# Kernel tuning notes

Hardware: AMD Instinct MI355X
Metric: run time of the kernel (lower is better)

The kernel has to match this reference:

```python
import jax, jax.numpy as jnp
import numpy as np

B, T, C, H = 4, 4096, 1024, 64

def setup_inputs() -> dict:
    key = jax.random.key(0)
    k1, k2, k3, k4 = jax.random.split(key, 4)
    x = jax.random.normal(k1, (B, T, C), dtype=jnp.float32)
    # Linear(n_embed, head_size, bias=False), stored as [in, out] for x @ W
    s = 1.0 / np.sqrt(C)
    Wq = jax.random.uniform(k2, (C, H), dtype=jnp.float32, minval=-s, maxval=s)
    Wk = jax.random.uniform(k3, (C, H), dtype=jnp.float32, minval=-s, maxval=s)
    Wv = jax.random.uniform(k4, (C, H), dtype=jnp.float32, minval=-s, maxval=s)
    return {"x": x, "Wq": Wq, "Wk": Wk, "Wv": Wv}

def reference(x, Wq, Wk, Wv):
    Bn, Tn, Cn = x.shape
    q = x @ Wq  # [B,T,H]
    k = x @ Wk  # [B,T,H]
    v = x @ Wv  # [B,T,H]
    # NOTE: original scales by C**-0.5 (embedding dim), not head_size**-0.5
    wei = jnp.einsum('bqh,bkh->bqk', q, k) * (Cn ** -0.5)  # [B,T,T]
    causal = jnp.tril(jnp.ones((Tn, Tn), dtype=bool))
    wei = jnp.where(causal, wei, -jnp.inf)
    wei = jax.nn.softmax(wei, axis=-1)
    out = jnp.einsum('bqk,bkh->bqh', wei, v)  # [B,T,H]
    return out
```

## Files before the change

### kernel.cpp

```cpp
#include <hip/hip_runtime.h>
#include <hip/hip_bf16.h>


#define B_DIM 4
#define T_DIM 4096
#define C_DIM 1024
#define H_DIM 64
#define SCALE2 0.0450842066f
#define KP 72

typedef __attribute__((ext_vector_type(8))) short bf8;
typedef __attribute__((ext_vector_type(4))) float f32x4;

__device__ __forceinline__ float fast_exp2(float f) {
    return __builtin_amdgcn_exp2f(f);
}
__device__ __forceinline__ ushort f2bf(float f) {
    union { float f; uint u; } x; x.f = f;
    const uint u = x.u;
    return (ushort)((u + 0x7FFFu + ((u >> 16) & 1u)) >> 16);
}
__device__ __forceinline__ uint cvt_pk_bf16(float lo, float hi) {
    uint r;
    asm("v_cvt_pk_bf16_f32 %0, %1, %2" : "=v"(r) : "v"(lo), "v"(hi));
    return r;
}

__global__ __launch_bounds__(256) void wt_kernel(
    const float* __restrict__ Wq, const float* __restrict__ Wk,
    const float* __restrict__ Wv, ushort* __restrict__ wtg)
{
    const int id  = blockIdx.x * 256 + threadIdx.x;
    const int col = id >> 7;
    const int k8  = (id & 127) * 8;
    const int m   = col >> 6, lc = col & 63;
    const float* W = (m == 0) ? Wq : (m == 1) ? Wk : Wv;
    ushort o[8];
    #pragma unroll
    for (int i = 0; i < 8; ++i)
        o[i] = f2bf(W[(size_t)(k8 + i) * H_DIM + lc]);
    *(bf8*)&wtg[(size_t)col * C_DIM + k8] = *(bf8*)o;
}

__global__ __launch_bounds__(256) void qkv_mfma_kernel(
    const float* __restrict__ x, const ushort* __restrict__ wtg,
    ushort* __restrict__ qo, ushort* __restrict__ ko, ushort* __restrict__ vo)
{
    __shared__ ushort xs[32][KP];
    __shared__ ushort wts[192][KP];
    const int t    = threadIdx.x;
    const int lane = t & 63, wave = t >> 6;
    const int g    = lane >> 4, lid = lane & 15;
    const size_t r0 = (size_t)blockIdx.x * 32;

    f32x4 acc[2][3] = {};

    const int xrow = t >> 3, xcol = (t & 7) * 8;
    float4 xr[2];
    bf8 wreg[6];

    xr[0] = *(const float4*)&x[(r0 + xrow) * C_DIM + xcol];
    xr[1] = *(const float4*)&x[(r0 + xrow) * C_DIM + xcol + 4];
    #pragma unroll
    for (int it = 0; it < 6; ++it) {
        const int n = t + it * 256;
        wreg[it] = *(const bf8*)&wtg[(size_t)(n >> 3) * C_DIM + (n & 7) * 8];
    }

    for (int kc = 0; kc < C_DIM / 64; ++kc) {
        __syncthreads();
        {
            uint p[4];
            p[0] = cvt_pk_bf16(xr[0].x, xr[0].y); p[1] = cvt_pk_bf16(xr[0].z, xr[0].w);
            p[2] = cvt_pk_bf16(xr[1].x, xr[1].y); p[3] = cvt_pk_bf16(xr[1].z, xr[1].w);
            *(bf8*)&xs[xrow][xcol] = *(bf8*)p;
            #pragma unroll
            for (int it = 0; it < 6; ++it) {
                const int n = t + it * 256;
                *(bf8*)&wts[n >> 3][(n & 7) * 8] = wreg[it];
            }
        }
        __syncthreads();
        if (kc + 1 < C_DIM / 64) {
            const int kb = (kc + 1) * 64;
            xr[0] = *(const float4*)&x[(r0 + xrow) * C_DIM + kb + xcol];
            xr[1] = *(const float4*)&x[(r0 + xrow) * C_DIM + kb + xcol + 4];
            #pragma unroll
            for (int it = 0; it < 6; ++it) {
                const int n = t + it * 256;
                wreg[it] = *(const bf8*)&wtg[(size_t)(n >> 3) * C_DIM + kb + (n & 7) * 8];
            }
        }
        #pragma unroll
        for (int ks = 0; ks < 2; ++ks) {
            const bf8 a0 = *(const bf8*)&xs[lid][ks * 32 + g * 8];
            const bf8 a1 = *(const bf8*)&xs[16 + lid][ks * 32 + g * 8];
            #pragma unroll
            for (int j = 0; j < 3; ++j) {
                const int ct = wave * 3 + j;
                const bf8 bb = *(const bf8*)&wts[ct * 16 + lid][ks * 32 + g * 8];
                acc[0][j] = __builtin_amdgcn_mfma_f32_16x16x32_bf16(a0, bb, acc[0][j], 0, 0, 0);
                acc[1][j] = __builtin_amdgcn_mfma_f32_16x16x32_bf16(a1, bb, acc[1][j], 0, 0, 0);
            }
        }
    }

    #pragma unroll
    for (int rt = 0; rt < 2; ++rt)
        #pragma unroll
        for (int j = 0; j < 3; ++j) {
            const int ct = wave * 3 + j;
            const int m  = ct >> 2, lc = (ct & 3) * 16 + lid;
            ushort* dst = (m == 0) ? qo : (m == 1) ? ko : vo;
            const float sc = (m == 0) ? SCALE2 : 1.f;
            #pragma unroll
            for (int r = 0; r < 4; ++r) {
                const size_t row = r0 + rt * 16 + 4 * g + r;
                dst[row * H_DIM + lc] = f2bf(acc[rt][j][r] * sc);
            }
        }
}

__global__ __launch_bounds__(256) void flash_mfma_kernel(
    const ushort* __restrict__ q, const ushort* __restrict__ k,
    const ushort* __restrict__ v, float* __restrict__ pO,
    float* __restrict__ pm, float* __restrict__ pl,
    float* __restrict__ out, int S, int nslots, int direct)
{
    const int qt = 63 - blockIdx.y;
    const int c  = blockIdx.x;
    const int kt_begin = c * S;
    const int kt_end   = min((c + 1) * S, qt + 1);
    if (kt_begin >= kt_end) return;

    __shared__ ushort ks[64][KP];
    __shared__ ushort vt[64][KP];
    __shared__ ushort ps[4][16][KP];

    const int t    = threadIdx.x;
    const int lane = t & 63, wave = t >> 6;
    const int g    = lane >> 4, lid = lane & 15;
    const int b    = blockIdx.z;
    const int bq0  = qt * 64;
    const size_t base = (size_t)b * T_DIM * H_DIM;

    const size_t qoff = base + (size_t)(bq0 + wave * 16 + lid) * H_DIM;
    const bf8 qf0 = *(const bf8*)&q[qoff + g * 8];
    const bf8 qf1 = *(const bf8*)&q[qoff + 32 + g * 8];

    f32x4 o_acc[4] = {};
    float m_run = -1e30f, l_run = 0.f;

    const int krow = t >> 3, kcol = (t & 7) * 8;
    const int vj = (t & 31) * 2, vc = (t >> 5) * 8;
    bf8 kr0, kr1, vr0, vr1;
    {
        const int kg = kt_begin * 64;
        kr0 = *(const bf8*)&k[base + (size_t)(kg + krow) * H_DIM + kcol];
        kr1 = *(const bf8*)&k[base + (size_t)(kg + 32 + krow) * H_DIM + kcol];
        vr0 = *(const bf8*)&v[base + (size_t)(kg + vj) * H_DIM + vc];
        vr1 = *(const bf8*)&v[base + (size_t)(kg + vj + 1) * H_DIM + vc];
    }

    for (int kt64 = kt_begin; kt64 < kt_end; ++kt64) {
        __syncthreads();
        *(bf8*)&ks[krow][kcol]      = kr0;
        *(bf8*)&ks[32 + krow][kcol] = kr1;
        #pragma unroll
        for (int i = 0; i < 8; ++i) {
            const uint pk = (uint)(ushort)vr0[i] | ((uint)(ushort)vr1[i] << 16);
            *(uint*)&vt[vc + i][vj] = pk;
        }
        __syncthreads();
        if (kt64 + 1 < kt_end) {
            const int kg = (kt64 + 1) * 64;
            kr0 = *(const bf8*)&k[base + (size_t)(kg + krow) * H_DIM + kcol];
            kr1 = *(const bf8*)&k[base + (size_t)(kg + 32 + krow) * H_DIM + kcol];
            vr0 = *(const bf8*)&v[base + (size_t)(kg + vj) * H_DIM + vc];
            vr1 = *(const bf8*)&v[base + (size_t)(kg + vj + 1) * H_DIM + vc];
        }

        f32x4 st[4];
        #pragma unroll
        for (int kt = 0; kt < 4; ++kt) {
            const bf8 kf0 = *(const bf8*)&ks[kt * 16 + lid][g * 8];
            const bf8 kf1 = *(const bf8*)&ks[kt * 16 + lid][32 + g * 8];
            f32x4 a = {0.f, 0.f, 0.f, 0.f};
            a = __builtin_amdgcn_mfma_f32_16x16x32_bf16(kf0, qf0, a, 0, 0, 0);
            a = __builtin_amdgcn_mfma_f32_16x16x32_bf16(kf1, qf1, a, 0, 0, 0);
            st[kt] = a;
        }

        if (kt64 == qt) {
            const int qloc = wave * 16 + lid;
            #pragma unroll
            for (int kt = 0; kt < 4; ++kt)
                #pragma unroll
                for (int r = 0; r < 4; ++r)
                    if (kt * 16 + 4 * g + r > qloc) st[kt][r] = -1e30f;
        }

        float mx = fmaxf(fmaxf(fmaxf(st[0][0], st[0][1]), fmaxf(st[0][2], st[0][3])),
                   fmaxf(fmaxf(fmaxf(st[1][0], st[1][1]), fmaxf(st[1][2], st[1][3])),
                   fmaxf(fmaxf(fmaxf(st[2][0], st[2][1]), fmaxf(st[2][2], st[2][3])),
                         fmaxf(fmaxf(st[3][0], st[3][1]), fmaxf(st[3][2], st[3][3])))));
        mx = fmaxf(mx, __shfl_xor(mx, 16));
        mx = fmaxf(mx, __shfl_xor(mx, 32));
        const bool nof = (mx <= m_run + 8.0f);
        const float mnew = nof ? m_run : mx;
        const float fsc  = nof ? 1.0f : fast_exp2(m_run - mnew);
        m_run = mnew;
        float ls = 0.f;
        #pragma unroll
        for (int kt = 0; kt < 4; ++kt)
            #pragma unroll
            for (int r = 0; r < 4; ++r) {
                const float p = fast_exp2(st[kt][r] - mnew);
                st[kt][r] = p;
                ls += p;
            }
        ls += __shfl_xor(ls, 16);
        ls += __shfl_xor(ls, 32);
        l_run = l_run * fsc + ls;

        #pragma unroll
        for (int kt = 0; kt < 4; ++kt) {
            uint2 w;
            w.x = cvt_pk_bf16(st[kt][0], st[kt][1]);
            w.y = cvt_pk_bf16(st[kt][2], st[kt][3]);
            *(uint2*)&ps[wave][lid][kt * 16 + 4 * g] = w;
        }

        if (!__all(nof)) {
            float fb[4];
            #pragma unroll
            for (int r = 0; r < 4; ++r) fb[r] = __shfl(fsc, 4 * g + r);
            #pragma unroll
            for (int ht = 0; ht < 4; ++ht)
                #pragma unroll
                for (int r = 0; r < 4; ++r) o_acc[ht][r] *= fb[r];
        }

        const bf8 pa0 = *(const bf8*)&ps[wave][lid][g * 8];
        const bf8 pa1 = *(const bf8*)&ps[wave][lid][32 + g * 8];
        #pragma unroll
        for (int ht = 0; ht < 4; ++ht) {
            const bf8 vb0 = *(const bf8*)&vt[ht * 16 + lid][g * 8];
            const bf8 vb1 = *(const bf8*)&vt[ht * 16 + lid][32 + g * 8];
            o_acc[ht] = __builtin_amdgcn_mfma_f32_16x16x32_bf16(pa0, vb0, o_acc[ht], 0, 0, 0);
            o_acc[ht] = __builtin_amdgcn_mfma_f32_16x16x32_bf16(pa1, vb1, o_acc[ht], 0, 0, 0);
        }
    }

    if (direct) {
        float linv[4];
        #pragma unroll
        for (int r = 0; r < 4; ++r) linv[r] = 1.f / __shfl(l_run, 4 * g + r);
        #pragma unroll
        for (int r = 0; r < 4; ++r) {
            const size_t rowoff = base + (size_t)(bq0 + wave * 16 + 4 * g + r) * H_DIM;
            #pragma unroll
            for (int ht = 0; ht < 4; ++ht)
                out[rowoff + ht * 16 + lid] = o_acc[ht][r] * linv[r];
        }
    } else {
        const size_t u = ((size_t)b * 64 + qt) * nslots + c;
        #pragma unroll
        for (int r = 0; r < 4; ++r) {
            const int row = wave * 16 + 4 * g + r;
            #pragma unroll
            for (int ht = 0; ht < 4; ++ht)
                pO[u * 4096 + (size_t)row * 64 + ht * 16 + lid] = o_acc[ht][r];
        }
        if (g == 0) {
            pm[u * 64 + wave * 16 + lid] = m_run;
            pl[u * 64 + wave * 16 + lid] = l_run;
        }
    }
}

__global__ __launch_bounds__(256) void combine_kernel(
    const float* __restrict__ pO, const float* __restrict__ pm,
    const float* __restrict__ pl, float* __restrict__ out,
    int S, int nslots)
{
    const int qt = blockIdx.x, b = blockIdx.y;
    const int nch = min(nslots, (qt + S) / S);
    const int t = threadIdx.x;
    const int row = t >> 2, seg = (t & 3) * 16;
    const size_t u0 = ((size_t)b * 64 + qt) * nslots;

    float M = -1e30f;
    for (int c = 0; c < nch; ++c)
        M = fmaxf(M, pm[(u0 + c) * 64 + row]);
    float L = 0.f, alpha[8];
    for (int c = 0; c < nch; ++c) {
        alpha[c] = fast_exp2(pm[(u0 + c) * 64 + row] - M);
        L += pl[(u0 + c) * 64 + row] * alpha[c];
    }
    const float inv = 1.f / L;

    float4 o[4] = {};
    for (int c = 0; c < nch; ++c) {
        const float a = alpha[c];
        #pragma unroll
        for (int j = 0; j < 4; ++j) {
            const float4 p = *(const float4*)&pO[(u0 + c) * 4096 +
                                                 (size_t)row * 64 + seg + j * 4];
            o[j].x += p.x * a; o[j].y += p.y * a;
            o[j].z += p.z * a; o[j].w += p.w * a;
        }
    }
    const size_t ob = (size_t)b * T_DIM * H_DIM + (size_t)(qt * 64 + row) * H_DIM + seg;
    #pragma unroll
    for (int j = 0; j < 4; ++j) {
        float4 r;
        r.x = o[j].x * inv; r.y = o[j].y * inv;
        r.z = o[j].z * inv; r.w = o[j].w * inv;
        *(float4*)&out[ob + j * 4] = r;
    }
}

extern "C" void kernel_launch(void* const* d_in, const int* in_sizes, int n_in,
                              void* d_out, int out_size, void* d_ws, size_t ws_size,
                              hipStream_t stream)
{
    const float* x  = (const float*)d_in[0];
    const float* Wq = (const float*)d_in[1];
    const float* Wk = (const float*)d_in[2];
    const float* Wv = (const float*)d_in[3];
    float* out = (float*)d_out;

    const size_t MB = 1u << 20;
    char* ws = (char*)d_ws;
    ushort* qb  = (ushort*)(ws);
    ushort* kb  = (ushort*)(ws + 2 * MB);
    ushort* vb  = (ushort*)(ws + 4 * MB);
    ushort* wtg = (ushort*)(ws + 6 * MB);
    float*  pO  = (float*)(ws + 7 * MB);

    int nslots, S;
    if      (ws_size >= 41 * MB) { nslots = 8; S = 8;  }
    else if (ws_size >= 24 * MB) { nslots = 4; S = 16; }
    else if (ws_size >= 16 * MB) { nslots = 2; S = 32; }
    else                         { nslots = 1; S = 64; }
    const int direct = (nslots == 1);
    float* pm = pO + (size_t)nslots * 1048576;
    float* pl = pm + (size_t)nslots * 16384;

    hipLaunchKernelGGL(wt_kernel, dim3(96), dim3(256), 0, stream, Wq, Wk, Wv, wtg);
    hipLaunchKernelGGL(qkv_mfma_kernel, dim3((B_DIM * T_DIM) / 32), dim3(256),
                       0, stream, x, wtg, qb, kb, vb);
    hipLaunchKernelGGL(flash_mfma_kernel, dim3(nslots, 64, B_DIM), dim3(256),
                       0, stream, qb, kb, vb, pO, pm, pl, out, S, nslots, direct);
    if (!direct)
        hipLaunchKernelGGL(combine_kernel, dim3(64, B_DIM), dim3(256),
                           0, stream, pO, pm, pl, out, S, nslots);
}
```

Baseline: 77.16 us.

## Load MFMA weight and key fragments directly from global, double-buffer LDS tiles

In the QKV projection, weight fragments are now read from global memory straight into MFMA operand registers, so the 192-row weight LDS tile goes away. The x tile is double-buffered in LDS, which leaves one barrier per iteration instead of two. In the flash kernel, K fragments are also loaded directly from global into registers and the transposed V tile is double-buffered, again removing one barrier per key tile and the K staging. The cost is more register pressure and redundant, less coalesced global reads of K and the weights by each wave, which now depend on cache hits.

```diff
diff --git a/kernel.cpp b/kernel.cpp
--- a/kernel.cpp
+++ b/kernel.cpp
@@ -46,63 +46,65 @@
     const float* __restrict__ x, const ushort* __restrict__ wtg,
     ushort* __restrict__ qo, ushort* __restrict__ ko, ushort* __restrict__ vo)
 {
-    __shared__ ushort xs[32][KP];
-    __shared__ ushort wts[192][KP];
+    __shared__ ushort xs[2][32][KP];
     const int t    = threadIdx.x;
     const int lane = t & 63, wave = t >> 6;
     const int g    = lane >> 4, lid = lane & 15;
     const size_t r0 = (size_t)blockIdx.x * 32;
 
     f32x4 acc[2][3] = {};
-
     const int xrow = t >> 3, xcol = (t & 7) * 8;
     float4 xr[2];
-    bf8 wreg[6];
+    bf8 wf[2][3];
+
+    #define LOAD_WF(kc_) do { \
+        _Pragma("unroll") \
+        for (int ks = 0; ks < 2; ++ks) \
+            _Pragma("unroll") \
+            for (int j = 0; j < 3; ++j) { \
+                const int ct = wave * 3 + j; \
+                wf[ks][j] = *(const bf8*)&wtg[(size_t)(ct * 16 + lid) * C_DIM + \
+                                              (kc_) * 64 + ks * 32 + g * 8]; \
+            } } while (0)
 
     xr[0] = *(const float4*)&x[(r0 + xrow) * C_DIM + xcol];
     xr[1] = *(const float4*)&x[(r0 + xrow) * C_DIM + xcol + 4];
-    #pragma unroll
-    for (int it = 0; it < 6; ++it) {
-        const int n = t + it * 256;
-        wreg[it] = *(const bf8*)&wtg[(size_t)(n >> 3) * C_DIM + (n & 7) * 8];
-    }
-
+    LOAD_WF(0);
+    {
+        uint p[4];
+        p[0] = cvt_pk_bf16(xr[0].x, xr[0].y); p[1] = cvt_pk_bf16(xr[0].z, xr[0].w);
+        p[2] = cvt_pk_bf16(xr[1].x, xr[1].y); p[3] = cvt_pk_bf16(xr[1].z, xr[1].w);
+        *(bf8*)&xs[0][xrow][xcol] = *(bf8*)p;
+    }
+    xr[0] = *(const float4*)&x[(r0 + xrow) * C_DIM + 64 + xcol];
+    xr[1] = *(const float4*)&x[(r0 + xrow) * C_DIM + 64 + xcol + 4];
+    __syncthreads();
+
+    int cur = 0;
     for (int kc = 0; kc < C_DIM / 64; ++kc) {
-        __syncthreads();
-        {
+        #pragma unroll
+        for (int ks = 0; ks < 2; ++ks) {
+            const bf8 a0 = *(const bf8*)&xs[cur][lid][ks * 32 + g * 8];
+            const bf8 a1 = *(const bf8*)&xs[cur][16 + lid][ks * 32 + g * 8];
+            #pragma unroll
+            for (int j = 0; j < 3; ++j) {
+                acc[0][j] = __builtin_amdgcn_mfma_f32_16x16x32_bf16(a0, wf[ks][j], acc[0][j], 0, 0, 0);
+                acc[1][j] = __builtin_amdgcn_mfma_f32_16x16x32_bf16(a1, wf[ks][j], acc[1][j], 0, 0, 0);
+            }
+        }
+        if (kc + 1 < C_DIM / 64) {
+            LOAD_WF(kc + 1);
             uint p[4];
             p[0] = cvt_pk_bf16(xr[0].x, xr[0].y); p[1] = cvt_pk_bf16(xr[0].z, xr[0].w);
             p[2] = cvt_pk_bf16(xr[1].x, xr[1].y); p[3] = cvt_pk_bf16(xr[1].z, xr[1].w);
-            *(bf8*)&xs[xrow][xcol] = *(bf8*)p;
-            #pragma unroll
-            for (int it = 0; it < 6; ++it) {
-                const int n = t + it * 256;
-                *(bf8*)&wts[n >> 3][(n & 7) * 8] = wreg[it];
+            *(bf8*)&xs[cur ^ 1][xrow][xcol] = *(bf8*)p;
+            if (kc + 2 < C_DIM / 64) {
+                xr[0] = *(const float4*)&x[(r0 + xrow) * C_DIM + (kc + 2) * 64 + xcol];
+                xr[1] = *(const float4*)&x[(r0 + xrow) * C_DIM + (kc + 2) * 64 + xcol + 4];
             }
         }
         __syncthreads();
-        if (kc + 1 < C_DIM / 64) {
-            const int kb = (kc + 1) * 64;
-            xr[0] = *(const float4*)&x[(r0 + xrow) * C_DIM + kb + xcol];
-            xr[1] = *(const float4*)&x[(r0 + xrow) * C_DIM + kb + xcol + 4];
-            #pragma unroll
-            for (int it = 0; it < 6; ++it) {
-                const int n = t + it * 256;
-                wreg[it] = *(const bf8*)&wtg[(size_t)(n >> 3) * C_DIM + kb + (n & 7) * 8];
-            }
-        }
-        #pragma unroll
-        for (int ks = 0; ks < 2; ++ks) {
-            const bf8 a0 = *(const bf8*)&xs[lid][ks * 32 + g * 8];
-            const bf8 a1 = *(const bf8*)&xs[16 + lid][ks * 32 + g * 8];
-            #pragma unroll
-            for (int j = 0; j < 3; ++j) {
-                const int ct = wave * 3 + j;
-                const bf8 bb = *(const bf8*)&wts[ct * 16 + lid][ks * 32 + g * 8];
-                acc[0][j] = __builtin_amdgcn_mfma_f32_16x16x32_bf16(a0, bb, acc[0][j], 0, 0, 0);
-                acc[1][j] = __builtin_amdgcn_mfma_f32_16x16x32_bf16(a1, bb, acc[1][j], 0, 0, 0);
-            }
-        }
+        cur ^= 1;
     }
 
     #pragma unroll
@@ -119,6 +121,7 @@
                 dst[row * H_DIM + lc] = f2bf(acc[rt][j][r] * sc);
             }
         }
+    #undef LOAD_WF
 }
 
 __global__ __launch_bounds__(256) void flash_mfma_kernel(
@@ -133,8 +136,7 @@
     const int kt_end   = min((c + 1) * S, qt + 1);
     if (kt_begin >= kt_end) return;
 
-    __shared__ ushort ks[64][KP];
-    __shared__ ushort vt[64][KP];
+    __shared__ ushort vtbuf[2][64][KP];
     __shared__ ushort ps[4][16][KP];
 
     const int t    = threadIdx.x;
@@ -143,6 +145,7 @@
     const int b    = blockIdx.z;
     const int bq0  = qt * 64;
     const size_t base = (size_t)b * T_DIM * H_DIM;
+    const ushort* kbase = k + base;
 
     const size_t qoff = base + (size_t)(bq0 + wave * 16 + lid) * H_DIM;
     const bf8 qf0 = *(const bf8*)&q[qoff + g * 8];
@@ -151,44 +154,59 @@
     f32x4 o_acc[4] = {};
     float m_run = -1e30f, l_run = 0.f;
 
-    const int krow = t >> 3, kcol = (t & 7) * 8;
+    bf8 kf0[4], kf1[4];
+    #define LOAD_KF(kg0_) do { \
+        _Pragma("unroll") \
+        for (int kt = 0; kt < 4; ++kt) { \
+            const size_t koff = (size_t)((kg0_) + kt * 16 + lid) * H_DIM; \
+            kf0[kt] = *(const bf8*)&kbase[koff + g * 8]; \
+            kf1[kt] = *(const bf8*)&kbase[koff + 32 + g * 8]; \
+        } } while (0)
+
     const int vj = (t & 31) * 2, vc = (t >> 5) * 8;
-    bf8 kr0, kr1, vr0, vr1;
+    bf8 vr0, vr1;
+
+    LOAD_KF(kt_begin * 64);
     {
         const int kg = kt_begin * 64;
-        kr0 = *(const bf8*)&k[base + (size_t)(kg + krow) * H_DIM + kcol];
-        kr1 = *(const bf8*)&k[base + (size_t)(kg + 32 + krow) * H_DIM + kcol];
         vr0 = *(const bf8*)&v[base + (size_t)(kg + vj) * H_DIM + vc];
         vr1 = *(const bf8*)&v[base + (size_t)(kg + vj + 1) * H_DIM + vc];
     }
-
+    #pragma unroll
+    for (int i = 0; i < 8; ++i) {
+        const uint pk = (uint)(ushort)vr0[i] | ((uint)(ushort)vr1[i] << 16);
+        *(uint*)&vtbuf[0][vc + i][vj] = pk;
+    }
+    if (kt_begin + 1 < kt_end) {
+        const int kg = (kt_begin + 1) * 64;
+        vr0 = *(const bf8*)&v[base + (size_t)(kg + vj) * H_DIM + vc];
+        vr1 = *(const bf8*)&v[base + (size_t)(kg + vj + 1) * H_DIM + vc];
+    }
+    __syncthreads();
+
+    int cur = 0;
     for (int kt64 = kt_begin; kt64 < kt_end; ++kt64) {
-        __syncthreads();
-        *(bf8*)&ks[krow][kcol]      = kr0;
-        *(bf8*)&ks[32 + krow][kcol] = kr1;
-        #pragma unroll
-        for (int i = 0; i < 8; ++i) {
-            const uint pk = (uint)(ushort)vr0[i] | ((uint)(ushort)vr1[i] << 16);
-            *(uint*)&vt[vc + i][vj] = pk;
-        }
-        __syncthreads();
+        f32x4 st[4];
+        #pragma unroll
+        for (int kt = 0; kt < 4; ++kt) {
+            f32x4 a = {0.f, 0.f, 0.f, 0.f};
+            a = __builtin_amdgcn_mfma_f32_16x16x32_bf16(kf0[kt], qf0, a, 0, 0, 0);
+            a = __builtin_amdgcn_mfma_f32_16x16x32_bf16(kf1[kt], qf1, a, 0, 0, 0);
+            st[kt] = a;
+        }
+        if (kt64 + 1 < kt_end) LOAD_KF((kt64 + 1) * 64);
+
         if (kt64 + 1 < kt_end) {
-            const int kg = (kt64 + 1) * 64;
-            kr0 = *(const bf8*)&k[base + (size_t)(kg + krow) * H_DIM + kcol];
-            kr1 = *(const bf8*)&k[base + (size_t)(kg + 32 + krow) * H_DIM + kcol];
-            vr0 = *(const bf8*)&v[base + (size_t)(kg + vj) * H_DIM + vc];
-            vr1 = *(const bf8*)&v[base + (size_t)(kg + vj + 1) * H_DIM + vc];
-        }
-
-        f32x4 st[4];
-        #pragma unroll
-        for (int kt = 0; kt < 4; ++kt) {
-            const bf8 kf0 = *(const bf8*)&ks[kt * 16 + lid][g * 8];
-            const bf8 kf1 = *(const bf8*)&ks[kt * 16 + lid][32 + g * 8];
-            f32x4 a = {0.f, 0.f, 0.f, 0.f};
-            a = __builtin_amdgcn_mfma_f32_16x16x32_bf16(kf0, qf0, a, 0, 0, 0);
-            a = __builtin_amdgcn_mfma_f32_16x16x32_bf16(kf1, qf1, a, 0, 0, 0);
-            st[kt] = a;
+            #pragma unroll
+            for (int i = 0; i < 8; ++i) {
+                const uint pk = (uint)(ushort)vr0[i] | ((uint)(ushort)vr1[i] << 16);
+                *(uint*)&vtbuf[cur ^ 1][vc + i][vj] = pk;
+            }
+            if (kt64 + 2 < kt_end) {
+                const int kg = (kt64 + 2) * 64;
+                vr0 = *(const bf8*)&v[base + (size_t)(kg + vj) * H_DIM + vc];
+                vr1 = *(const bf8*)&v[base + (size_t)(kg + vj + 1) * H_DIM + vc];
+            }
         }
 
         if (kt64 == qt) {
@@ -245,12 +263,16 @@
         const bf8 pa1 = *(const bf8*)&ps[wave][lid][32 + g * 8];
         #pragma unroll
         for (int ht = 0; ht < 4; ++ht) {
-            const bf8 vb0 = *(const bf8*)&vt[ht * 16 + lid][g * 8];
-            const bf8 vb1 = *(const bf8*)&vt[ht * 16 + lid][32 + g * 8];
+            const bf8 vb0 = *(const bf8*)&vtbuf[cur][ht * 16 + lid][g * 8];
+            const bf8 vb1 = *(const bf8*)&vtbuf[cur][ht * 16 + lid][32 + g * 8];
             o_acc[ht] = __builtin_amdgcn_mfma_f32_16x16x32_bf16(pa0, vb0, o_acc[ht], 0, 0, 0);
             o_acc[ht] = __builtin_amdgcn_mfma_f32_16x16x32_bf16(pa1, vb1, o_acc[ht], 0, 0, 0);
         }
-    }
+
+        __syncthreads();
+        cur ^= 1;
+    }
+    #undef LOAD_KF
 
     if (direct) {
         float linv[4];
```

Measured after the change: 123.1 us. 1.6x slower.

## Switch flash attention to 32x32 MFMA with 128-row query tiles and register-resident P

Applied to the files above, without the earlier changes.

The attention kernel now processes 128 query rows per block (32 per wave) with 32x32x16 bf16 MFMA instead of 16x16x32. The P matrix is repacked in registers with v_permlane32_swap instead of a round-trip through shared memory, and K/V tiles are reused across twice as many query rows. The causal tail skips compute per wave. Combine and partial buffers are re-indexed for the new tile size. This raises register pressure and halves the number of query-tile blocks, which may reduce occupancy and parallelism.

```diff
diff --git a/kernel.cpp b/kernel.cpp
--- a/kernel.cpp
+++ b/kernel.cpp
@@ -11,6 +11,7 @@
 
 typedef __attribute__((ext_vector_type(8))) short bf8;
 typedef __attribute__((ext_vector_type(4))) float f32x4;
+typedef __attribute__((ext_vector_type(16))) float f32x16;
 
 __device__ __forceinline__ float fast_exp2(float f) {
     return __builtin_amdgcn_exp2f(f);
@@ -24,6 +25,17 @@
     uint r;
     asm("v_cvt_pk_bf16_f32 %0, %1, %2" : "=v"(r) : "v"(lo), "v"(hi));
     return r;
+}
+__device__ __forceinline__ void permswapf(float& a, float& b) {
+    asm volatile("v_permlane32_swap_b32 %0, %1" : "+v"(a), "+v"(b));
+}
+__device__ __forceinline__ void permswapu(uint& a, uint& b) {
+    asm volatile("v_permlane32_swap_b32 %0, %1" : "+v"(a), "+v"(b));
+}
+__device__ __forceinline__ bf8 frag_from(uint w0, uint w1, uint w2, uint w3) {
+    union { uint u[4]; bf8 f; } x;
+    x.u[0] = w0; x.u[1] = w1; x.u[2] = w2; x.u[3] = w3;
+    return x.f;
 }
 
 __global__ __launch_bounds__(256) void wt_kernel(
@@ -127,45 +139,62 @@
     float* __restrict__ pm, float* __restrict__ pl,
     float* __restrict__ out, int S, int nslots, int direct)
 {
-    const int qt = 63 - blockIdx.y;
-    const int c  = blockIdx.x;
+    const int qt  = 31 - blockIdx.y;
+    const int c   = blockIdx.x;
+    const int ntk = 2 * qt + 2;
     const int kt_begin = c * S;
-    const int kt_end   = min((c + 1) * S, qt + 1);
+    const int kt_end   = min((c + 1) * S, ntk);
     if (kt_begin >= kt_end) return;
 
     __shared__ ushort ks[64][KP];
     __shared__ ushort vt[64][KP];
-    __shared__ ushort ps[4][16][KP];
+    __shared__ float  fsh[4][32];
+    __shared__ float  lsh[4][32];
 
     const int t    = threadIdx.x;
     const int lane = t & 63, wave = t >> 6;
-    const int g    = lane >> 4, lid = lane & 15;
+    const int l31  = lane & 31, hi = lane >> 5;
     const int b    = blockIdx.z;
-    const int bq0  = qt * 64;
+    const int bq0  = qt * 128;
+    const int qrow0 = bq0 + wave * 32;
+    const int ktw_max = (qrow0 + 31) >> 6;
     const size_t base = (size_t)b * T_DIM * H_DIM;
 
-    const size_t qoff = base + (size_t)(bq0 + wave * 16 + lid) * H_DIM;
-    const bf8 qf0 = *(const bf8*)&q[qoff + g * 8];
-    const bf8 qf1 = *(const bf8*)&q[qoff + 32 + g * 8];
-
-    f32x4 o_acc[4] = {};
-    float m_run = -1e30f, l_run = 0.f;
-
-    const int krow = t >> 3, kcol = (t & 7) * 8;
+    bf8 qf[4];
+    {
+        const size_t qoff = base + (size_t)(qrow0 + l31) * H_DIM + hi * 8;
+        #pragma unroll
+        for (int kk = 0; kk < 4; ++kk)
+            qf[kk] = *(const bf8*)&q[qoff + kk * 16];
+    }
+
+    f32x16 oa0 = {}, oa1 = {};
+    float m_run = -1e29f, l_run = 0.f;
+
+    const int krow = t >> 2, kc16 = (t & 3) * 16;
     const int vj = (t & 31) * 2, vc = (t >> 5) * 8;
     bf8 kr0, kr1, vr0, vr1;
     {
         const int kg = kt_begin * 64;
-        kr0 = *(const bf8*)&k[base + (size_t)(kg + krow) * H_DIM + kcol];
-        kr1 = *(const bf8*)&k[base + (size_t)(kg + 32 + krow) * H_DIM + kcol];
+        kr0 = *(const bf8*)&k[base + (size_t)(kg + krow) * H_DIM + kc16];
+        kr1 = *(const bf8*)&k[base + (size_t)(kg + krow) * H_DIM + kc16 + 8];
         vr0 = *(const bf8*)&v[base + (size_t)(kg + vj) * H_DIM + vc];
         vr1 = *(const bf8*)&v[base + (size_t)(kg + vj + 1) * H_DIM + vc];
     }
 
+    #define BUILD_PA(dst, sv, bofs) do {                                   \
+        uint a0_ = cvt_pk_bf16(sv[(bofs)+0], sv[(bofs)+1]);                \
+        uint b0_ = cvt_pk_bf16(sv[(bofs)+4], sv[(bofs)+5]);                \
+        uint a1_ = cvt_pk_bf16(sv[(bofs)+2], sv[(bofs)+3]);                \
+        uint b1_ = cvt_pk_bf16(sv[(bofs)+6], sv[(bofs)+7]);                \
+        permswapu(a0_, b0_); permswapu(a1_, b1_);                          \
+        dst = frag_from(a0_, a1_, b0_, b1_);                               \
+    } while (0)
+
     for (int kt64 = kt_begin; kt64 < kt_end; ++kt64) {
         __syncthreads();
-        *(bf8*)&ks[krow][kcol]      = kr0;
-        *(bf8*)&ks[32 + krow][kcol] = kr1;
+        *(bf8*)&ks[krow][kc16]     = kr0;
+        *(bf8*)&ks[krow][kc16 + 8] = kr1;
         #pragma unroll
         for (int i = 0; i < 8; ++i) {
             const uint pk = (uint)(ushort)vr0[i] | ((uint)(ushort)vr1[i] << 16);
@@ -174,107 +203,107 @@
         __syncthreads();
         if (kt64 + 1 < kt_end) {
             const int kg = (kt64 + 1) * 64;
-            kr0 = *(const bf8*)&k[base + (size_t)(kg + krow) * H_DIM + kcol];
-            kr1 = *(const bf8*)&k[base + (size_t)(kg + 32 + krow) * H_DIM + kcol];
+            kr0 = *(const bf8*)&k[base + (size_t)(kg + krow) * H_DIM + kc16];
+            kr1 = *(const bf8*)&k[base + (size_t)(kg + krow) * H_DIM + kc16 + 8];
             vr0 = *(const bf8*)&v[base + (size_t)(kg + vj) * H_DIM + vc];
             vr1 = *(const bf8*)&v[base + (size_t)(kg + vj + 1) * H_DIM + vc];
         }
-
-        f32x4 st[4];
-        #pragma unroll
-        for (int kt = 0; kt < 4; ++kt) {
-            const bf8 kf0 = *(const bf8*)&ks[kt * 16 + lid][g * 8];
-            const bf8 kf1 = *(const bf8*)&ks[kt * 16 + lid][32 + g * 8];
-            f32x4 a = {0.f, 0.f, 0.f, 0.f};
-            a = __builtin_amdgcn_mfma_f32_16x16x32_bf16(kf0, qf0, a, 0, 0, 0);
-            a = __builtin_amdgcn_mfma_f32_16x16x32_bf16(kf1, qf1, a, 0, 0, 0);
-            st[kt] = a;
-        }
-
-        if (kt64 == qt) {
-            const int qloc = wave * 16 + lid;
-            #pragma unroll
-            for (int kt = 0; kt < 4; ++kt)
-                #pragma unroll
-                for (int r = 0; r < 4; ++r)
-                    if (kt * 16 + 4 * g + r > qloc) st[kt][r] = -1e30f;
-        }
-
-        float mx = fmaxf(fmaxf(fmaxf(st[0][0], st[0][1]), fmaxf(st[0][2], st[0][3])),
-                   fmaxf(fmaxf(fmaxf(st[1][0], st[1][1]), fmaxf(st[1][2], st[1][3])),
-                   fmaxf(fmaxf(fmaxf(st[2][0], st[2][1]), fmaxf(st[2][2], st[2][3])),
-                         fmaxf(fmaxf(st[3][0], st[3][1]), fmaxf(st[3][2], st[3][3])))));
-        mx = fmaxf(mx, __shfl_xor(mx, 16));
-        mx = fmaxf(mx, __shfl_xor(mx, 32));
+        if (kt64 > ktw_max) continue;
+
+        f32x16 st0 = {}, st1 = {};
+        #pragma unroll
+        for (int kk = 0; kk < 4; ++kk) {
+            const bf8 kfa = *(const bf8*)&ks[l31][kk * 16 + hi * 8];
+            st0 = __builtin_amdgcn_mfma_f32_32x32x16_bf16(kfa, qf[kk], st0, 0, 0, 0);
+        }
+        #pragma unroll
+        for (int kk = 0; kk < 4; ++kk) {
+            const bf8 kfb = *(const bf8*)&ks[32 + l31][kk * 16 + hi * 8];
+            st1 = __builtin_amdgcn_mfma_f32_32x32x16_bf16(kfb, qf[kk], st1, 0, 0, 0);
+        }
+
+        if (kt64 * 64 + 63 > qrow0) {
+            const int qg  = qrow0 + l31;
+            const int kb0 = kt64 * 64 + 4 * hi;
+            #pragma unroll
+            for (int r = 0; r < 16; ++r) {
+                const int key0 = kb0 + (r & 3) + 8 * (r >> 2);
+                if (key0 > qg)      st0[r] = -1e30f;
+                if (key0 + 32 > qg) st1[r] = -1e30f;
+            }
+        }
+
+        float mx = st0[0];
+        #pragma unroll
+        for (int r = 1; r < 16; ++r) mx = fmaxf(mx, st0[r]);
+        #pragma unroll
+        for (int r = 0; r < 16; ++r) mx = fmaxf(mx, st1[r]);
+        { float ma = mx, mb = mx; permswapf(ma, mb); mx = fmaxf(ma, mb); }
         const bool nof = (mx <= m_run + 8.0f);
         const float mnew = nof ? m_run : mx;
         const float fsc  = nof ? 1.0f : fast_exp2(m_run - mnew);
         m_run = mnew;
         float ls = 0.f;
         #pragma unroll
-        for (int kt = 0; kt < 4; ++kt)
-            #pragma unroll
-            for (int r = 0; r < 4; ++r) {
-                const float p = fast_exp2(st[kt][r] - mnew);
-                st[kt][r] = p;
-                ls += p;
-            }
-        ls += __shfl_xor(ls, 16);
-        ls += __shfl_xor(ls, 32);
+        for (int r = 0; r < 16; ++r) { st0[r] = fast_exp2(st0[r] - mnew); ls += st0[r]; }
+        #pragma unroll
+        for (int r = 0; r < 16; ++r) { st1[r] = fast_exp2(st1[r] - mnew); ls += st1[r]; }
+        { float la = ls, lb = ls; permswapf(la, lb); ls = la + lb; }
         l_run = l_run * fsc + ls;
 
-        #pragma unroll
-        for (int kt = 0; kt < 4; ++kt) {
-            uint2 w;
-            w.x = cvt_pk_bf16(st[kt][0], st[kt][1]);
-            w.y = cvt_pk_bf16(st[kt][2], st[kt][3]);
-            *(uint2*)&ps[wave][lid][kt * 16 + 4 * g] = w;
-        }
+        bf8 pa[4];
+        BUILD_PA(pa[0], st0, 0);
+        BUILD_PA(pa[1], st0, 8);
+        BUILD_PA(pa[2], st1, 0);
+        BUILD_PA(pa[3], st1, 8);
 
         if (!__all(nof)) {
-            float fb[4];
-            #pragma unroll
-            for (int r = 0; r < 4; ++r) fb[r] = __shfl(fsc, 4 * g + r);
-            #pragma unroll
-            for (int ht = 0; ht < 4; ++ht)
-                #pragma unroll
-                for (int r = 0; r < 4; ++r) o_acc[ht][r] *= fb[r];
-        }
-
-        const bf8 pa0 = *(const bf8*)&ps[wave][lid][g * 8];
-        const bf8 pa1 = *(const bf8*)&ps[wave][lid][32 + g * 8];
-        #pragma unroll
-        for (int ht = 0; ht < 4; ++ht) {
-            const bf8 vb0 = *(const bf8*)&vt[ht * 16 + lid][g * 8];
-            const bf8 vb1 = *(const bf8*)&vt[ht * 16 + lid][32 + g * 8];
-            o_acc[ht] = __builtin_amdgcn_mfma_f32_16x16x32_bf16(pa0, vb0, o_acc[ht], 0, 0, 0);
-            o_acc[ht] = __builtin_amdgcn_mfma_f32_16x16x32_bf16(pa1, vb1, o_acc[ht], 0, 0, 0);
-        }
-    }
+            if (lane < 32) fsh[wave][l31] = fsc;
+            #pragma unroll
+            for (int j = 0; j < 4; ++j) {
+                const float4 fb = *(const float4*)&fsh[wave][8 * j + 4 * hi];
+                oa0[4*j+0] *= fb.x; oa0[4*j+1] *= fb.y; oa0[4*j+2] *= fb.z; oa0[4*j+3] *= fb.w;
+                oa1[4*j+0] *= fb.x; oa1[4*j+1] *= fb.y; oa1[4*j+2] *= fb.z; oa1[4*j+3] *= fb.w;
+            }
+        }
+
+        #pragma unroll
+        for (int kk = 0; kk < 4; ++kk) {
+            const bf8 vb0 = *(const bf8*)&vt[l31][kk * 16 + hi * 8];
+            const bf8 vb1 = *(const bf8*)&vt[32 + l31][kk * 16 + hi * 8];
+            oa0 = __builtin_amdgcn_mfma_f32_32x32x16_bf16(pa[kk], vb0, oa0, 0, 0, 0);
+            oa1 = __builtin_amdgcn_mfma_f32_32x32x16_bf16(pa[kk], vb1, oa1, 0, 0, 0);
+        }
+    }
+    #undef BUILD_PA
 
     if (direct) {
-        float linv[4];
-        #pragma unroll
-        for (int r = 0; r < 4; ++r) linv[r] = 1.f / __shfl(l_run, 4 * g + r);
-        #pragma unroll
-        for (int r = 0; r < 4; ++r) {
-            const size_t rowoff = base + (size_t)(bq0 + wave * 16 + 4 * g + r) * H_DIM;
-            #pragma unroll
-            for (int ht = 0; ht < 4; ++ht)
-                out[rowoff + ht * 16 + lid] = o_acc[ht][r] * linv[r];
+        if (lane < 32) lsh[wave][l31] = l_run;
+        #pragma unroll
+        for (int j = 0; j < 4; ++j) {
+            const float4 lv = *(const float4*)&lsh[wave][8 * j + 4 * hi];
+            const float iv[4] = {1.f / lv.x, 1.f / lv.y, 1.f / lv.z, 1.f / lv.w};
+            #pragma unroll
+            for (int rr = 0; rr < 4; ++rr) {
+                const size_t rowoff = base + (size_t)(qrow0 + 8 * j + 4 * hi + rr) * H_DIM;
+                out[rowoff + l31]      = oa0[4 * j + rr] * iv[rr];
+                out[rowoff + 32 + l31] = oa1[4 * j + rr] * iv[rr];
+            }
         }
     } else {
-        const size_t u = ((size_t)b * 64 + qt) * nslots + c;
-        #pragma unroll
-        for (int r = 0; r < 4; ++r) {
-            const int row = wave * 16 + 4 * g + r;
-            #pragma unroll
-            for (int ht = 0; ht < 4; ++ht)
-                pO[u * 4096 + (size_t)row * 64 + ht * 16 + lid] = o_acc[ht][r];
-        }
-        if (g == 0) {
-            pm[u * 64 + wave * 16 + lid] = m_run;
-            pl[u * 64 + wave * 16 + lid] = l_run;
+        const size_t u = ((size_t)b * 32 + qt) * nslots + c;
+        float* po = pO + u * 8192;
+        #pragma unroll
+        for (int j = 0; j < 4; ++j)
+            #pragma unroll
+            for (int rr = 0; rr < 4; ++rr) {
+                const int row = wave * 32 + 8 * j + 4 * hi + rr;
+                po[(size_t)row * 64 + l31]      = oa0[4 * j + rr];
+                po[(size_t)row * 64 + 32 + l31] = oa1[4 * j + rr];
+            }
+        if (lane < 32) {
+            pm[u * 128 + wave * 32 + l31] = m_run;
+            pl[u * 128 + wave * 32 + l31] = l_run;
         }
     }
 }
@@ -285,35 +314,36 @@
     int S, int nslots)
 {
     const int qt = blockIdx.x, b = blockIdx.y;
-    const int nch = min(nslots, (qt + S) / S);
+    const int ntk = 2 * qt + 2;
+    const int nch = min(nslots, (ntk + S - 1) / S);
     const int t = threadIdx.x;
-    const int row = t >> 2, seg = (t & 3) * 16;
-    const size_t u0 = ((size_t)b * 64 + qt) * nslots;
+    const int row = t >> 1, seg = (t & 1) * 32;
+    const size_t u0 = ((size_t)b * 32 + qt) * nslots;
 
     float M = -1e30f;
-    for (int c = 0; c < nch; ++c)
-        M = fmaxf(M, pm[(u0 + c) * 64 + row]);
+    for (int cc = 0; cc < nch; ++cc)
+        M = fmaxf(M, pm[(u0 + cc) * 128 + row]);
     float L = 0.f, alpha[8];
-    for (int c = 0; c < nch; ++c) {
-        alpha[c] = fast_exp2(pm[(u0 + c) * 64 + row] - M);
-        L += pl[(u0 + c) * 64 + row] * alpha[c];
+    for (int cc = 0; cc < nch; ++cc) {
+        alpha[cc] = fast_exp2(pm[(u0 + cc) * 128 + row] - M);
+        L += pl[(u0 + cc) * 128 + row] * alpha[cc];
     }
     const float inv = 1.f / L;
 
-    float4 o[4] = {};
-    for (int c = 0; c < nch; ++c) {
-        const float a = alpha[c];
-        #pragma unroll
-        for (int j = 0; j < 4; ++j) {
-            const float4 p = *(const float4*)&pO[(u0 + c) * 4096 +
+    float4 o[8] = {};
+    for (int cc = 0; cc < nch; ++cc) {
+        const float a = alpha[cc];
+        #pragma unroll
+        for (int j = 0; j < 8; ++j) {
+            const float4 p = *(const float4*)&pO[(u0 + cc) * 8192 +
                                                  (size_t)row * 64 + seg + j * 4];
             o[j].x += p.x * a; o[j].y += p.y * a;
             o[j].z += p.z * a; o[j].w += p.w * a;
         }
     }
-    const size_t ob = (size_t)b * T_DIM * H_DIM + (size_t)(qt * 64 + row) * H_DIM + seg;
+    const size_t ob = (size_t)b * T_DIM * H_DIM + (size_t)(qt * 128 + row) * H_DIM + seg;
     #pragma unroll
-    for (int j = 0; j < 4; ++j) {
+    for (int j = 0; j < 8; ++j) {
         float4 r;
         r.x = o[j].x * inv; r.y = o[j].y * inv;
         r.z = o[j].z * inv; r.w = o[j].w * inv;
@@ -351,9 +381,9 @@
     hipLaunchKernelGGL(wt_kernel, dim3(96), dim3(256), 0, stream, Wq, Wk, Wv, wtg);
     hipLaunchKernelGGL(qkv_mfma_kernel, dim3((B_DIM * T_DIM) / 32), dim3(256),
                        0, stream, x, wtg, qb, kb, vb);
-    hipLaunchKernelGGL(flash_mfma_kernel, dim3(nslots, 64, B_DIM), dim3(256),
+    hipLaunchKernelGGL(flash_mfma_kernel, dim3(nslots, T_DIM / 128, B_DIM), dim3(256),
                        0, stream, qb, kb, vb, pO, pm, pl, out, S, nslots, direct);
     if (!direct)
-        hipLaunchKernelGGL(combine_kernel, dim3(64, B_DIM), dim3(256),
+        hipLaunchKernelGGL(combine_kernel, dim3(T_DIM / 128, B_DIM), dim3(256),
                            0, stream, pO, pm, pl, out, S, nslots);
 }
```

Result: no change. 77.59 us (+0.6%).
